# Kernel tuning notes

Measured on AMD Instinct MI355X. Metric: run time of the kernel, lower is better.

The kernel has to match this reference:

```python
import jax, jax.numpy as jnp
import numpy as np

B, C_IN, H, W = 4, 128, 32, 32
C_SKIP, C_OUT = 64, 64
D_MODEL = 2 * C_SKIP            # 128 (channels after concat)
D_STATE, D_CONV, EXPAND = 16, 4, 2
D_INNER = EXPAND * D_MODEL      # 256
DT_RANK = int(np.ceil(D_MODEL / 16))  # 8
LN_EPS = 1e-5


def setup_inputs() -> dict:
    key = jax.random.key(0)
    ks = jax.random.split(key, 12)
    s = 0.02
    return {
        "x": jax.random.normal(ks[0], (B, C_IN, H, W), jnp.float32),
        "skip_x": jax.random.normal(ks[1], (B, C_SKIP, 2 * H, 2 * W), jnp.float32),
        # ConvTranspose2d(in, skip, k=2, s=2): torch weight layout (in, out, kh, kw)
        "up_w": jax.random.normal(ks[2], (C_IN, C_SKIP, 2, 2), jnp.float32) * s,
        "up_b": jnp.zeros((C_SKIP,), jnp.float32),
        # Mamba params (torch Linear layout: (out_features, in_features))
        "in_proj_w": jax.random.normal(ks[3], (2 * D_INNER, D_MODEL), jnp.float32) * s,
        "conv1d_w": jax.random.normal(ks[4], (D_INNER, 1, D_CONV), jnp.float32) * s,
        "conv1d_b": jnp.zeros((D_INNER,), jnp.float32),
        "x_proj_w": jax.random.normal(ks[5], (DT_RANK + 2 * D_STATE, D_INNER), jnp.float32) * s,
        "dt_proj_w": jax.random.normal(ks[6], (D_INNER, DT_RANK), jnp.float32) * s,
        "dt_proj_b": jnp.zeros((D_INNER,), jnp.float32),
        "A_log": jnp.log(jnp.broadcast_to(jnp.arange(1, D_STATE + 1, dtype=jnp.float32), (D_INNER, D_STATE))),
        "Dp": jnp.ones((D_INNER,), jnp.float32),
        "out_proj_w": jax.random.normal(ks[7], (D_MODEL, D_INNER), jnp.float32) * s,
        "ln_gamma": jnp.ones((D_MODEL,), jnp.float32),
        "ln_beta": jnp.zeros((D_MODEL,), jnp.float32),
        # Conv2d 1x1 (out, in)
        "convout_w": jax.random.normal(ks[8], (C_OUT, D_MODEL), jnp.float32) * s,
        "convout_b": jnp.zeros((C_OUT,), jnp.float32),
    }


def _selective_scan(u, delta, A, Bm, Cm, Dp):
    # u, delta: (B,L,Din); A: (Din,Ds); Bm, Cm: (B,L,Ds)
    deltaA = jnp.exp(delta[..., None] * A)                        # (B,L,Din,Ds)
    deltaBu = delta[..., None] * Bm[:, :, None, :] * u[..., None]  # (B,L,Din,Ds)

    def step(h, xs):
        dA, dBu, c = xs                 # (B,Din,Ds),(B,Din,Ds),(B,Ds)
        h = dA * h + dBu
        y = jnp.einsum('bdn,bn->bd', h, c)
        return h, y

    h0 = jnp.zeros((u.shape[0], D_INNER, D_STATE), u.dtype)
    xs = (deltaA.transpose(1, 0, 2, 3), deltaBu.transpose(1, 0, 2, 3), Cm.transpose(1, 0, 2))
    _, ys = jax.lax.scan(step, h0, xs)  # (L,B,Din)
    return ys.transpose(1, 0, 2) + u * Dp


def _mamba(seq, in_proj_w, conv1d_w, conv1d_b, x_proj_w, dt_proj_w, dt_proj_b, A_log, Dp, out_proj_w):
    # seq: (B, L, D_MODEL)
    xz = seq @ in_proj_w.T                      # (B,L,2*Din)
    u, z = jnp.split(xz, 2, axis=-1)
    # depthwise causal conv1d along L
    uc = u.transpose(0, 2, 1)                   # (B,Din,L)
    uc = jax.lax.conv_general_dilated(
        uc, conv1d_w, window_strides=(1,), padding=[(D_CONV - 1, 0)],
        feature_group_count=D_INNER, dimension_numbers=('NCH', 'OIH', 'NCH'))
    uc = uc + conv1d_b[None, :, None]
    u = jax.nn.silu(uc.transpose(0, 2, 1))      # (B,L,Din)
    dbc = u @ x_proj_w.T                        # (B,L,DT_RANK+2*Ds)
    dt, Bm, Cm = jnp.split(dbc, [DT_RANK, DT_RANK + D_STATE], axis=-1)
    delta = jax.nn.softplus(dt @ dt_proj_w.T + dt_proj_b)
    A = -jnp.exp(A_log)
    y = _selective_scan(u, delta, A, Bm, Cm, Dp)
    y = y * jax.nn.silu(z)
    return y @ out_proj_w.T                     # (B,L,D_MODEL)


def reference(x, skip_x, up_w, up_b, in_proj_w, conv1d_w, conv1d_b, x_proj_w,
              dt_proj_w, dt_proj_b, A_log, Dp, out_proj_w, ln_gamma, ln_beta,
              convout_w, convout_b):
    b, _, h, w = x.shape
    # ConvTranspose2d k=2 s=2: each pixel expands to a 2x2 block
    up = jnp.einsum('bchw,coij->bohiwj', x, up_w).reshape(b, C_SKIP, 2 * h, 2 * w)
    up = up + up_b[None, :, None, None]
    xc = jnp.concatenate([up, skip_x], axis=1)  # (B, D_MODEL, 2H, 2W)
    Hh, Ww = xc.shape[2], xc.shape[3]
    seq = xc.reshape(b, D_MODEL, Hh * Ww).transpose(0, 2, 1)  # (B,L,D)
    y = _mamba(seq, in_proj_w, conv1d_w, conv1d_b, x_proj_w, dt_proj_w,
               dt_proj_b, A_log, Dp, out_proj_w)
    xm = y.transpose(0, 2, 1).reshape(b, D_MODEL, Hh, Ww)
    # permute -> LayerNorm over channels -> permute back
    xn = xm.transpose(0, 2, 3, 1)
    mu = xn.mean(-1, keepdims=True)
    var = xn.var(-1, keepdims=True)
    xn = (xn - mu) * jax.lax.rsqrt(var + LN_EPS) * ln_gamma + ln_beta
    xm = jax.nn.silu(xn.transpose(0, 3, 1, 2))
    out = jnp.einsum('bchw,oc->bohw', xm, convout_w) + convout_b[None, :, None, None]
    return out
```

## Files before the change

### kernel.cpp

```cpp
#include <hip/hip_runtime.h>

#define L_SEQ 4096
#define DM 128
#define DIN 256
#define NC 128
#define CHUNK 32

__global__ __launch_bounds__(256) void upcat_kernel(
    const float* __restrict__ x, const float* __restrict__ skip,
    const float* __restrict__ up_w, const float* __restrict__ up_b,
    float* __restrict__ seq) {
  int b = blockIdx.x >> 6, hh = blockIdx.x & 63;
  int h = hh >> 1, i = hh & 1;
  int tid = threadIdx.x;
  __shared__ float xs[128][32];
  __shared__ float wsh[2][128][64];
  for (int e = tid; e < 1024; e += 256) {
    int c = e >> 3, q = e & 7;
    *(float4*)&xs[c][q * 4] =
        *(const float4*)(x + (((size_t)b * 128 + c) * 32 + h) * 32 + q * 4);
  }
  for (int e = tid; e < 8192; e += 256) {
    int c = e >> 6, o = e & 63;
    float2 v = *(const float2*)(up_w + c * 256 + o * 4 + i * 2);
    wsh[0][c][o] = v.x;
    wsh[1][c][o] = v.y;
  }
  __syncthreads();
  int tx = tid & 15, ty = tid >> 4;
  float4 bv = *(const float4*)(up_b + tx * 4);
  float acc[4][4];
#pragma unroll
  for (int a = 0; a < 4; ++a) {
    acc[a][0] = bv.x; acc[a][1] = bv.y; acc[a][2] = bv.z; acc[a][3] = bv.w;
  }
#pragma unroll 4
  for (int c = 0; c < 128; ++c) {
    float x0 = xs[c][ty * 2];
    float x1 = xs[c][ty * 2 + 1];
    float4 w0 = *(const float4*)&wsh[0][c][tx * 4];
    float4 w1 = *(const float4*)&wsh[1][c][tx * 4];
    acc[0][0] = fmaf(x0, w0.x, acc[0][0]); acc[0][1] = fmaf(x0, w0.y, acc[0][1]);
    acc[0][2] = fmaf(x0, w0.z, acc[0][2]); acc[0][3] = fmaf(x0, w0.w, acc[0][3]);
    acc[1][0] = fmaf(x0, w1.x, acc[1][0]); acc[1][1] = fmaf(x0, w1.y, acc[1][1]);
    acc[1][2] = fmaf(x0, w1.z, acc[1][2]); acc[1][3] = fmaf(x0, w1.w, acc[1][3]);
    acc[2][0] = fmaf(x1, w0.x, acc[2][0]); acc[2][1] = fmaf(x1, w0.y, acc[2][1]);
    acc[2][2] = fmaf(x1, w0.z, acc[2][2]); acc[2][3] = fmaf(x1, w0.w, acc[2][3]);
    acc[3][0] = fmaf(x1, w1.x, acc[3][0]); acc[3][1] = fmaf(x1, w1.y, acc[3][1]);
    acc[3][2] = fmaf(x1, w1.z, acc[3][2]); acc[3][3] = fmaf(x1, w1.w, acc[3][3]);
  }
  size_t mrow_base = (size_t)b * L_SEQ + (size_t)hh * 64;
#pragma unroll
  for (int a = 0; a < 4; ++a) {
    int ww = ty * 4 + a;
    *(float4*)(seq + (mrow_base + ww) * DM + tx * 4) =
        make_float4(acc[a][0], acc[a][1], acc[a][2], acc[a][3]);
  }
  for (int e = tid; e < 4096; e += 256) {
    int c = e & 63, ww = e >> 6;
    seq[(mrow_base + ww) * DM + 64 + c] =
        skip[((size_t)b * 64 + c) * (size_t)L_SEQ + hh * 64 + ww];
  }
}

__global__ __launch_bounds__(256) void gemm_bt128(
    const float* __restrict__ A, const float* __restrict__ W,
    float* __restrict__ C, int M, int N, int K) {
  __shared__ float As[32][132];
  __shared__ float Ws[32][68];
  int m0 = blockIdx.x * 128, n0 = blockIdx.y * 64;
  int tid = threadIdx.x;
  int tx = tid & 15, ty = tid >> 4;
  float acc[8][4];
#pragma unroll
  for (int a = 0; a < 8; ++a)
#pragma unroll
    for (int bb = 0; bb < 4; ++bb) acc[a][bb] = 0.f;

  for (int k0 = 0; k0 < K; k0 += 32) {
    __syncthreads();
    for (int e = tid; e < 1024; e += 256) {
      int r = e >> 3, c4 = (e & 7) << 2;
      float4 va = *(const float4*)(A + (size_t)(m0 + r) * K + k0 + c4);
      As[c4 + 0][r] = va.x; As[c4 + 1][r] = va.y;
      As[c4 + 2][r] = va.z; As[c4 + 3][r] = va.w;
    }
    for (int e = tid; e < 512; e += 256) {
      int r = e >> 3, c4 = (e & 7) << 2;
      float4 vw = *(const float4*)(W + (size_t)(n0 + r) * K + k0 + c4);
      Ws[c4 + 0][r] = vw.x; Ws[c4 + 1][r] = vw.y;
      Ws[c4 + 2][r] = vw.z; Ws[c4 + 3][r] = vw.w;
    }
    __syncthreads();
#pragma unroll
    for (int kk = 0; kk < 32; ++kk) {
      float4 a0 = *(const float4*)(&As[kk][ty * 8]);
      float4 a1 = *(const float4*)(&As[kk][ty * 8 + 4]);
      float4 wv = *(const float4*)(&Ws[kk][tx * 4]);
      float a_[8] = {a0.x, a0.y, a0.z, a0.w, a1.x, a1.y, a1.z, a1.w};
      float w_[4] = {wv.x, wv.y, wv.z, wv.w};
#pragma unroll
      for (int a = 0; a < 8; ++a)
#pragma unroll
        for (int bb = 0; bb < 4; ++bb)
          acc[a][bb] = fmaf(a_[a], w_[bb], acc[a][bb]);
    }
  }
#pragma unroll
  for (int a = 0; a < 8; ++a)
#pragma unroll
    for (int bb = 0; bb < 4; ++bb)
      C[(size_t)(m0 + ty * 8 + a) * N + n0 + tx * 4 + bb] = acc[a][bb];
}

__global__ __launch_bounds__(256) void xproj_kernel(
    const float* __restrict__ xz, const float* __restrict__ cw,
    const float* __restrict__ cb, const float* __restrict__ W,
    float* __restrict__ dbc, float* __restrict__ u_out) {
  __shared__ float xzt[67][64];
  __shared__ float us[64][68];
  int m0 = blockIdx.x * 64;
  int tid = threadIdx.x;
  int lane = tid & 63;
  int w = __builtin_amdgcn_readfirstlane(tid >> 6);
  int jbase = blockIdx.y * 20 + w * 5;
  const float* Wb = W + jbase * 256;
  bool first = (m0 & (L_SEQ - 1)) == 0;
  int cc4 = (tid & 15) << 2;
  int r0 = tid >> 4;
  float acc[5];
#pragma unroll
  for (int j = 0; j < 5; ++j) acc[j] = 0.f;
  for (int k0 = 0; k0 < 256; k0 += 64) {
    __syncthreads();
    for (int e = tid; e < 67 * 16; e += 256) {
      int rr = e >> 4, c4 = (e & 15) << 2;
      float4 v;
      if (first && rr < 3)
        v = make_float4(0.f, 0.f, 0.f, 0.f);
      else
        v = *(const float4*)(xz + (size_t)(m0 - 3 + rr) * 512 + k0 + c4);
      *(float4*)&xzt[rr][c4] = v;
    }
    __syncthreads();
    {
      int d = k0 + cc4;
      float4 cw0 = *(const float4*)(cw + (d + 0) * 4);
      float4 cw1 = *(const float4*)(cw + (d + 1) * 4);
      float4 cw2 = *(const float4*)(cw + (d + 2) * 4);
      float4 cw3 = *(const float4*)(cw + (d + 3) * 4);
      float4 cbv = *(const float4*)(cb + d);
#pragma unroll
      for (int s = 0; s < 4; ++s) {
        int r = r0 + s * 16;
        float a0 = cbv.x, a1 = cbv.y, a2 = cbv.z, a3 = cbv.w;
        a0 = fmaf(xzt[r + 0][cc4 + 0], cw0.x, a0);
        a0 = fmaf(xzt[r + 1][cc4 + 0], cw0.y, a0);
        a0 = fmaf(xzt[r + 2][cc4 + 0], cw0.z, a0);
        a0 = fmaf(xzt[r + 3][cc4 + 0], cw0.w, a0);
        a1 = fmaf(xzt[r + 0][cc4 + 1], cw1.x, a1);
        a1 = fmaf(xzt[r + 1][cc4 + 1], cw1.y, a1);
        a1 = fmaf(xzt[r + 2][cc4 + 1], cw1.z, a1);
        a1 = fmaf(xzt[r + 3][cc4 + 1], cw1.w, a1);
        a2 = fmaf(xzt[r + 0][cc4 + 2], cw2.x, a2);
        a2 = fmaf(xzt[r + 1][cc4 + 2], cw2.y, a2);
        a2 = fmaf(xzt[r + 2][cc4 + 2], cw2.z, a2);
        a2 = fmaf(xzt[r + 3][cc4 + 2], cw2.w, a2);
        a3 = fmaf(xzt[r + 0][cc4 + 3], cw3.x, a3);
        a3 = fmaf(xzt[r + 1][cc4 + 3], cw3.y, a3);
        a3 = fmaf(xzt[r + 2][cc4 + 3], cw3.z, a3);
        a3 = fmaf(xzt[r + 3][cc4 + 3], cw3.w, a3);
        float o0 = a0 / (1.f + __expf(-a0));
        float o1 = a1 / (1.f + __expf(-a1));
        float o2 = a2 / (1.f + __expf(-a2));
        float o3 = a3 / (1.f + __expf(-a3));
        *(float4*)&us[r][cc4] = make_float4(o0, o1, o2, o3);
        if (blockIdx.y == 0)
          *(float4*)(u_out + (size_t)(m0 + r) * 256 + d) =
              make_float4(o0, o1, o2, o3);
      }
    }
    __syncthreads();
#pragma unroll
    for (int kk = 0; kk < 64; kk += 4) {
      float4 a4 = *(const float4*)&us[lane][kk];
      float a_[4] = {a4.x, a4.y, a4.z, a4.w};
#pragma unroll
      for (int i = 0; i < 4; ++i)
#pragma unroll
        for (int j = 0; j < 5; ++j)
          acc[j] = fmaf(a_[i], Wb[j * 256 + k0 + kk + i], acc[j]);
    }
  }
  size_t base = (size_t)(m0 + lane) * 40 + jbase;
#pragma unroll
  for (int j = 0; j < 5; ++j) dbc[base + j] = acc[j];
}

__device__ __forceinline__ float softplus_f(float a) {
  return (a > 20.f) ? a : log1pf(__expf(a));
}

__global__ __launch_bounds__(256) void scan_pass1(
    const float* __restrict__ u, const float* __restrict__ dbc,
    const float* __restrict__ A_log, const float* __restrict__ Wdt,
    const float* __restrict__ bdt, float* __restrict__ carryA,
    float* __restrict__ carryH) {
  int bid = blockIdx.x;
  int b = bid >> 7;
  int c = bid & (NC - 1);
  int d = threadIdx.x;
  __shared__ float ls[CHUNK * 40];
  size_t l0 = (size_t)b * L_SEQ + (size_t)c * CHUNK;
  const float* rp = dbc + l0 * 40;
  for (int e = d; e < CHUNK * 40; e += 256) ls[e] = rp[e];
  float Ac[16];
  {
    const float4* ar = (const float4*)(A_log + d * 16);
#pragma unroll
    for (int q = 0; q < 4; ++q) {
      float4 v = ar[q];
      Ac[q * 4 + 0] = -__expf(v.x); Ac[q * 4 + 1] = -__expf(v.y);
      Ac[q * 4 + 2] = -__expf(v.z); Ac[q * 4 + 3] = -__expf(v.w);
    }
  }
  float wdt[8];
  {
    const float4* wr = (const float4*)(Wdt + d * 8);
    float4 v0 = wr[0], v1 = wr[1];
    wdt[0] = v0.x; wdt[1] = v0.y; wdt[2] = v0.z; wdt[3] = v0.w;
    wdt[4] = v1.x; wdt[5] = v1.y; wdt[6] = v1.z; wdt[7] = v1.w;
  }
  float bdt_v = bdt[d];
  const float* up = u + l0 * 256 + d;
  __syncthreads();
  float h[16];
#pragma unroll
  for (int n = 0; n < 16; ++n) h[n] = 0.f;
  float dvs = 0.f;
#pragma unroll 4
  for (int li = 0; li < CHUNK; ++li) {
    float uv = up[(size_t)li * 256];
    float acc = bdt_v;
#pragma unroll
    for (int j = 0; j < 8; ++j)
      acc = fmaf(ls[li * 40 + j], wdt[j], acc);
    float dv = softplus_f(acc);
    dvs += dv;
    float t = dv * uv;
#pragma unroll
    for (int n = 0; n < 16; ++n) {
      float dA = __expf(dv * Ac[n]);
      h[n] = fmaf(dA, h[n], t * ls[li * 40 + 8 + n]);
    }
  }
  float4* cA = (float4*)(carryA + ((size_t)bid * 256 + d) * 16);
  float4* cH = (float4*)(carryH + ((size_t)bid * 256 + d) * 16);
#pragma unroll
  for (int q = 0; q < 4; ++q) {
    cA[q] = make_float4(__expf(dvs * Ac[q * 4]), __expf(dvs * Ac[q * 4 + 1]),
                        __expf(dvs * Ac[q * 4 + 2]), __expf(dvs * Ac[q * 4 + 3]));
    cH[q] = make_float4(h[q * 4], h[q * 4 + 1], h[q * 4 + 2], h[q * 4 + 3]);
  }
}

__global__ __launch_bounds__(64) void scan_mid(
    const float* __restrict__ carryA, float* __restrict__ carryH) {
  int gid = blockIdx.x * 64 + threadIdx.x;
  int b = gid >> 12;
  int dn = gid & 4095;
  size_t i = ((size_t)(b * NC) << 12) + dn;
  float h = 0.f;
  float a = carryA[i], hl = carryH[i];
#pragma unroll 4
  for (int c = 0; c < NC - 1; ++c) {
    size_t i2 = i + 4096;
    float a2 = carryA[i2];
    float hl2 = carryH[i2];
    carryH[i] = h;
    h = fmaf(a, h, hl);
    a = a2; hl = hl2; i = i2;
  }
  carryH[i] = h;
}

__global__ __launch_bounds__(256) void scan_pass3(
    const float* __restrict__ u, const float* __restrict__ dbc,
    const float* __restrict__ xz, const float* __restrict__ A_log,
    const float* __restrict__ Wdt, const float* __restrict__ bdt,
    const float* __restrict__ Dp, const float* __restrict__ carryH,
    float* __restrict__ y) {
  int bid = blockIdx.x;
  int b = bid >> 7;
  int c = bid & (NC - 1);
  int d = threadIdx.x;
  __shared__ float ls[CHUNK * 40];
  size_t l0 = (size_t)b * L_SEQ + (size_t)c * CHUNK;
  const float* rp = dbc + l0 * 40;
  for (int e = d; e < CHUNK * 40; e += 256) ls[e] = rp[e];
  float Ac[16];
  {
    const float4* ar = (const float4*)(A_log + d * 16);
#pragma unroll
    for (int q = 0; q < 4; ++q) {
      float4 v = ar[q];
      Ac[q * 4 + 0] = -__expf(v.x); Ac[q * 4 + 1] = -__expf(v.y);
      Ac[q * 4 + 2] = -__expf(v.z); Ac[q * 4 + 3] = -__expf(v.w);
    }
  }
  float wdt[8];
  {
    const float4* wr = (const float4*)(Wdt + d * 8);
    float4 v0 = wr[0], v1 = wr[1];
    wdt[0] = v0.x; wdt[1] = v0.y; wdt[2] = v0.z; wdt[3] = v0.w;
    wdt[4] = v1.x; wdt[5] = v1.y; wdt[6] = v1.z; wdt[7] = v1.w;
  }
  float bdt_v = bdt[d];
  float Dv = Dp[d];
  float h[16];
  {
    const float4* cH = (const float4*)(carryH + ((size_t)bid * 256 + d) * 16);
#pragma unroll
    for (int q = 0; q < 4; ++q) {
      float4 v = cH[q];
      h[q * 4 + 0] = v.x; h[q * 4 + 1] = v.y;
      h[q * 4 + 2] = v.z; h[q * 4 + 3] = v.w;
    }
  }
  const float* up = u + l0 * 256 + d;
  const float* zp = xz + l0 * 512 + 256 + d;
  float* yp = y + l0 * 256 + d;
  __syncthreads();
#pragma unroll 4
  for (int li = 0; li < CHUNK; ++li) {
    float uv = up[(size_t)li * 256];
    float zv = zp[(size_t)li * 512];
    float acc = bdt_v;
#pragma unroll
    for (int j = 0; j < 8; ++j)
      acc = fmaf(ls[li * 40 + j], wdt[j], acc);
    float dv = softplus_f(acc);
    float t = dv * uv;
    float p = 0.f;
#pragma unroll
    for (int n = 0; n < 16; ++n) {
      float dA = __expf(dv * Ac[n]);
      h[n] = fmaf(dA, h[n], t * ls[li * 40 + 8 + n]);
      p = fmaf(h[n], ls[li * 40 + 24 + n], p);
    }
    float s = zv / (1.f + __expf(-zv));
    yp[(size_t)li * 256] = (p + uv * Dv) * s;
  }
}

__global__ __launch_bounds__(512) void fused_out_kernel(
    const float* __restrict__ y, const float* __restrict__ Wp,
    const float* __restrict__ gamma, const float* __restrict__ beta,
    const float* __restrict__ Wo, const float* __restrict__ bo,
    float* __restrict__ out) {
  __shared__ float As[32][68];
  __shared__ float Ws[32][132];
  __shared__ float xt[64][129];
  __shared__ float mus[64], invs[64];
  int tid = threadIdx.x;
  int m0 = blockIdx.x * 64;
  int tx = tid & 31, ty = tid >> 5;
  float acc[4][4];
#pragma unroll
  for (int a = 0; a < 4; ++a)
#pragma unroll
    for (int bb = 0; bb < 4; ++bb) acc[a][bb] = 0.f;

  for (int k0 = 0; k0 < 256; k0 += 32) {
    __syncthreads();
    {
      int e = tid;
      int r = e >> 3, c4 = (e & 7) << 2;
      float4 va = *(const float4*)(y + (size_t)(m0 + r) * 256 + k0 + c4);
      As[c4 + 0][r] = va.x; As[c4 + 1][r] = va.y;
      As[c4 + 2][r] = va.z; As[c4 + 3][r] = va.w;
    }
    for (int e = tid; e < 1024; e += 512) {
      int n = e >> 3, c4 = (e & 7) << 2;
      float4 vw = *(const float4*)(Wp + (size_t)n * 256 + k0 + c4);
      Ws[c4 + 0][n] = vw.x; Ws[c4 + 1][n] = vw.y;
      Ws[c4 + 2][n] = vw.z; Ws[c4 + 3][n] = vw.w;
    }
    __syncthreads();
#pragma unroll
    for (int kk = 0; kk < 32; ++kk) {
      float4 av = *(const float4*)(&As[kk][ty * 4]);
      float4 wv = *(const float4*)(&Ws[kk][tx * 4]);
      float a_[4] = {av.x, av.y, av.z, av.w};
      float w_[4] = {wv.x, wv.y, wv.z, wv.w};
#pragma unroll
      for (int a = 0; a < 4; ++a)
#pragma unroll
        for (int bb = 0; bb < 4; ++bb)
          acc[a][bb] = fmaf(a_[a], w_[bb], acc[a][bb]);
    }
  }
  __syncthreads();
#pragma unroll
  for (int a = 0; a < 4; ++a)
    *(float4*)&xt[ty * 4 + a][tx * 4] =
        make_float4(acc[a][0], acc[a][1], acc[a][2], acc[a][3]);
  __syncthreads();
  {
    int r = tid >> 3, kq = (tid & 7) * 16;
    float s = 0.f, q = 0.f;
#pragma unroll 8
    for (int kk = 0; kk < 16; ++kk) {
      float v = xt[r][kq + kk];
      s += v; q = fmaf(v, v, q);
    }
    s += __shfl_xor(s, 1, 64); s += __shfl_xor(s, 2, 64);
    s += __shfl_xor(s, 4, 64);
    q += __shfl_xor(q, 1, 64); q += __shfl_xor(q, 2, 64);
    q += __shfl_xor(q, 4, 64);
    if ((tid & 7) == 0) {
      float mu = s * (1.f / 128.f);
      float var = q * (1.f / 128.f) - mu * mu;
      mus[r] = mu;
      invs[r] = rsqrtf(var + 1e-5f);
    }
  }
  __syncthreads();
  for (int i = 0; i < 16; ++i) {
    int idx = tid + i * 512;
    int r = idx >> 7, k = idx & 127;
    float v = xt[r][k];
    float xn = (v - mus[r]) * invs[r] * gamma[k] + beta[k];
    xt[r][k] = xn / (1.f + __expf(-xn));
  }
  __syncthreads();
  int lane = tid & 63;
  int w = __builtin_amdgcn_readfirstlane(tid >> 6);
  int cbase = w * 8;
  const float* Wrow = Wo + cbase * 128;
  float acc2[8];
#pragma unroll
  for (int j = 0; j < 8; ++j) acc2[j] = 0.f;
#pragma unroll 4
  for (int k = 0; k < 128; ++k) {
    float v = xt[lane][k];
#pragma unroll
    for (int j = 0; j < 8; ++j)
      acc2[j] = fmaf(v, Wrow[j * 128 + k], acc2[j]);
  }
  int m = m0 + lane;
  int b = m >> 12, l = m & 4095;
#pragma unroll
  for (int j = 0; j < 8; ++j)
    out[((size_t)b * 64 + cbase + j) * 4096 + l] = acc2[j] + bo[cbase + j];
}

extern "C" void kernel_launch(void* const* d_in, const int* in_sizes, int n_in,
                              void* d_out, int out_size, void* d_ws, size_t ws_size,
                              hipStream_t stream) {
  (void)in_sizes; (void)n_in; (void)out_size; (void)ws_size;
  const float* x         = (const float*)d_in[0];
  const float* skip      = (const float*)d_in[1];
  const float* up_w      = (const float*)d_in[2];
  const float* up_b      = (const float*)d_in[3];
  const float* in_proj_w = (const float*)d_in[4];
  const float* conv1d_w  = (const float*)d_in[5];
  const float* conv1d_b  = (const float*)d_in[6];
  const float* x_proj_w  = (const float*)d_in[7];
  const float* dt_proj_w = (const float*)d_in[8];
  const float* dt_proj_b = (const float*)d_in[9];
  const float* A_log     = (const float*)d_in[10];
  const float* Dp        = (const float*)d_in[11];
  const float* out_proj_w= (const float*)d_in[12];
  const float* ln_gamma  = (const float*)d_in[13];
  const float* ln_beta   = (const float*)d_in[14];
  const float* convout_w = (const float*)d_in[15];
  const float* convout_b = (const float*)d_in[16];
  float* out = (float*)d_out;
  float* ws  = (float*)d_ws;

  float* seq    = ws;
  float* xz     = ws + 2097152;
  float* u      = ws + 10485760;
  float* dbc    = ws + 14680064;
  float* y      = ws + 15335424;
  float* carryA = ws + 19529728;
  float* carryH = ws + 21626880;

  upcat_kernel<<<256, 256, 0, stream>>>(x, skip, up_w, up_b, seq);
  gemm_bt128<<<dim3(16384 / 128, 512 / 64), 256, 0, stream>>>(
      seq, in_proj_w, xz, 16384, 512, 128);
  xproj_kernel<<<dim3(16384 / 64, 2), 256, 0, stream>>>(
      xz, conv1d_w, conv1d_b, x_proj_w, dbc, u);
  scan_pass1<<<4 * NC, 256, 0, stream>>>(u, dbc, A_log, dt_proj_w, dt_proj_b,
                                         carryA, carryH);
  scan_mid<<<256, 64, 0, stream>>>(carryA, carryH);
  scan_pass3<<<4 * NC, 256, 0, stream>>>(u, dbc, xz, A_log, dt_proj_w,
                                         dt_proj_b, Dp, carryH, y);
  fused_out_kernel<<<256, 512, 0, stream>>>(y, out_proj_w, ln_gamma, ln_beta,
                                            convout_w, convout_b, out);
}
```

Baseline: 201.5 us.

## Replace tiled SGEMMs with wave-uniform scalar-weight GEMMs for in_proj and out_proj

Both the in_proj GEMM and the out_proj part of the fused output kernel now use the same scheme. Each lane owns one row, whose activations are staged in LDS, and each wave owns 16 output columns whose weights are read as wave-uniform (scalar) loads. This removes the transposed LDS stores and the per-k-tile weight staging. The in_proj output goes through an LDS tile so the global stores stay coalesced. The trade-off is lower register blocking per thread (16 outputs against one activation per k), so arithmetic intensity per LDS read drops, which the scalar weight loads are meant to offset.

```diff
diff --git a/kernel.cpp b/kernel.cpp
--- a/kernel.cpp
+++ b/kernel.cpp
@@ -63,54 +63,47 @@
   }
 }
 
-__global__ __launch_bounds__(256) void gemm_bt128(
-    const float* __restrict__ A, const float* __restrict__ W,
-    float* __restrict__ C, int M, int N, int K) {
-  __shared__ float As[32][132];
-  __shared__ float Ws[32][68];
-  int m0 = blockIdx.x * 128, n0 = blockIdx.y * 64;
+__global__ __launch_bounds__(512) void inproj_kernel(
+    const float* __restrict__ seq, const float* __restrict__ W,
+    float* __restrict__ xz) {
+  __shared__ float us[64][133];
+  __shared__ float ot[64][129];
+  int m0 = blockIdx.x * 64;
+  int cb0 = blockIdx.y * 128;
   int tid = threadIdx.x;
-  int tx = tid & 15, ty = tid >> 4;
-  float acc[8][4];
-#pragma unroll
-  for (int a = 0; a < 8; ++a)
-#pragma unroll
-    for (int bb = 0; bb < 4; ++bb) acc[a][bb] = 0.f;
-
-  for (int k0 = 0; k0 < K; k0 += 32) {
-    __syncthreads();
-    for (int e = tid; e < 1024; e += 256) {
-      int r = e >> 3, c4 = (e & 7) << 2;
-      float4 va = *(const float4*)(A + (size_t)(m0 + r) * K + k0 + c4);
-      As[c4 + 0][r] = va.x; As[c4 + 1][r] = va.y;
-      As[c4 + 2][r] = va.z; As[c4 + 3][r] = va.w;
-    }
-    for (int e = tid; e < 512; e += 256) {
-      int r = e >> 3, c4 = (e & 7) << 2;
-      float4 vw = *(const float4*)(W + (size_t)(n0 + r) * K + k0 + c4);
-      Ws[c4 + 0][r] = vw.x; Ws[c4 + 1][r] = vw.y;
-      Ws[c4 + 2][r] = vw.z; Ws[c4 + 3][r] = vw.w;
-    }
-    __syncthreads();
-#pragma unroll
-    for (int kk = 0; kk < 32; ++kk) {
-      float4 a0 = *(const float4*)(&As[kk][ty * 8]);
-      float4 a1 = *(const float4*)(&As[kk][ty * 8 + 4]);
-      float4 wv = *(const float4*)(&Ws[kk][tx * 4]);
-      float a_[8] = {a0.x, a0.y, a0.z, a0.w, a1.x, a1.y, a1.z, a1.w};
-      float w_[4] = {wv.x, wv.y, wv.z, wv.w};
-#pragma unroll
-      for (int a = 0; a < 8; ++a)
-#pragma unroll
-        for (int bb = 0; bb < 4; ++bb)
-          acc[a][bb] = fmaf(a_[a], w_[bb], acc[a][bb]);
-    }
-  }
-#pragma unroll
-  for (int a = 0; a < 8; ++a)
-#pragma unroll
-    for (int bb = 0; bb < 4; ++bb)
-      C[(size_t)(m0 + ty * 8 + a) * N + n0 + tx * 4 + bb] = acc[a][bb];
+  int lane = tid & 63;
+  int w = __builtin_amdgcn_readfirstlane(tid >> 6);
+  const float* Wrow = W + (size_t)(cb0 + w * 16) * 128;
+#pragma unroll
+  for (int i = 0; i < 4; ++i) {
+    int e = tid + i * 512;
+    int r = e >> 5, cq = e & 31;
+    *(float4*)&us[r][cq * 4] =
+        *(const float4*)(seq + (size_t)(m0 + r) * 128 + cq * 4);
+  }
+  __syncthreads();
+  float acc[16];
+#pragma unroll
+  for (int j = 0; j < 16; ++j) acc[j] = 0.f;
+#pragma unroll 4
+  for (int k = 0; k < 128; ++k) {
+    float v = us[lane][k];
+#pragma unroll
+    for (int j = 0; j < 16; ++j)
+      acc[j] = fmaf(v, Wrow[j * 128 + k], acc[j]);
+  }
+#pragma unroll
+  for (int q = 0; q < 4; ++q)
+    *(float4*)&ot[lane][w * 16 + q * 4] =
+        make_float4(acc[q * 4], acc[q * 4 + 1], acc[q * 4 + 2], acc[q * 4 + 3]);
+  __syncthreads();
+#pragma unroll
+  for (int i = 0; i < 4; ++i) {
+    int e = tid + i * 512;
+    int r = e >> 5, cq = e & 31;
+    *(float4*)(xz + (size_t)(m0 + r) * 512 + cb0 + cq * 4) =
+        *(const float4*)&ot[r][cq * 4];
+  }
 }
 
 __global__ __launch_bounds__(256) void xproj_kernel(
@@ -358,53 +351,40 @@
     const float* __restrict__ gamma, const float* __restrict__ beta,
     const float* __restrict__ Wo, const float* __restrict__ bo,
     float* __restrict__ out) {
-  __shared__ float As[32][68];
-  __shared__ float Ws[32][132];
+  __shared__ float us[64][133];
   __shared__ float xt[64][129];
   __shared__ float mus[64], invs[64];
   int tid = threadIdx.x;
   int m0 = blockIdx.x * 64;
-  int tx = tid & 31, ty = tid >> 5;
-  float acc[4][4];
-#pragma unroll
-  for (int a = 0; a < 4; ++a)
-#pragma unroll
-    for (int bb = 0; bb < 4; ++bb) acc[a][bb] = 0.f;
-
-  for (int k0 = 0; k0 < 256; k0 += 32) {
+  int lane = tid & 63;
+  int w = __builtin_amdgcn_readfirstlane(tid >> 6);
+  float acc[16];
+#pragma unroll
+  for (int j = 0; j < 16; ++j) acc[j] = 0.f;
+  for (int kc = 0; kc < 256; kc += 128) {
     __syncthreads();
-    {
-      int e = tid;
-      int r = e >> 3, c4 = (e & 7) << 2;
-      float4 va = *(const float4*)(y + (size_t)(m0 + r) * 256 + k0 + c4);
-      As[c4 + 0][r] = va.x; As[c4 + 1][r] = va.y;
-      As[c4 + 2][r] = va.z; As[c4 + 3][r] = va.w;
-    }
-    for (int e = tid; e < 1024; e += 512) {
-      int n = e >> 3, c4 = (e & 7) << 2;
-      float4 vw = *(const float4*)(Wp + (size_t)n * 256 + k0 + c4);
-      Ws[c4 + 0][n] = vw.x; Ws[c4 + 1][n] = vw.y;
-      Ws[c4 + 2][n] = vw.z; Ws[c4 + 3][n] = vw.w;
+#pragma unroll
+    for (int i = 0; i < 4; ++i) {
+      int e = tid + i * 512;
+      int r = e >> 5, cq = e & 31;
+      *(float4*)&us[r][cq * 4] =
+          *(const float4*)(y + (size_t)(m0 + r) * 256 + kc + cq * 4);
     }
     __syncthreads();
-#pragma unroll
-    for (int kk = 0; kk < 32; ++kk) {
-      float4 av = *(const float4*)(&As[kk][ty * 4]);
-      float4 wv = *(const float4*)(&Ws[kk][tx * 4]);
-      float a_[4] = {av.x, av.y, av.z, av.w};
-      float w_[4] = {wv.x, wv.y, wv.z, wv.w};
-#pragma unroll
-      for (int a = 0; a < 4; ++a)
-#pragma unroll
-        for (int bb = 0; bb < 4; ++bb)
-          acc[a][bb] = fmaf(a_[a], w_[bb], acc[a][bb]);
-    }
-  }
-  __syncthreads();
-#pragma unroll
-  for (int a = 0; a < 4; ++a)
-    *(float4*)&xt[ty * 4 + a][tx * 4] =
-        make_float4(acc[a][0], acc[a][1], acc[a][2], acc[a][3]);
+    const float* Wrow = Wp + (size_t)(w * 16) * 256 + kc;
+#pragma unroll 4
+    for (int k = 0; k < 128; ++k) {
+      float v = us[lane][k];
+#pragma unroll
+      for (int j = 0; j < 16; ++j)
+        acc[j] = fmaf(v, Wrow[j * 256 + k], acc[j]);
+    }
+  }
+  __syncthreads();
+#pragma unroll
+  for (int q = 0; q < 4; ++q)
+    *(float4*)&xt[lane][w * 16 + q * 4] =
+        make_float4(acc[q * 4], acc[q * 4 + 1], acc[q * 4 + 2], acc[q * 4 + 3]);
   __syncthreads();
   {
     int r = tid >> 3, kq = (tid & 7) * 16;
@@ -434,10 +414,8 @@
     xt[r][k] = xn / (1.f + __expf(-xn));
   }
   __syncthreads();
-  int lane = tid & 63;
-  int w = __builtin_amdgcn_readfirstlane(tid >> 6);
   int cbase = w * 8;
-  const float* Wrow = Wo + cbase * 128;
+  const float* Wrow2 = Wo + cbase * 128;
   float acc2[8];
 #pragma unroll
   for (int j = 0; j < 8; ++j) acc2[j] = 0.f;
@@ -446,7 +424,7 @@
     float v = xt[lane][k];
 #pragma unroll
     for (int j = 0; j < 8; ++j)
-      acc2[j] = fmaf(v, Wrow[j * 128 + k], acc2[j]);
+      acc2[j] = fmaf(v, Wrow2[j * 128 + k], acc2[j]);
   }
   int m = m0 + lane;
   int b = m >> 12, l = m & 4095;
@@ -488,8 +466,7 @@
   float* carryH = ws + 21626880;
 
   upcat_kernel<<<256, 256, 0, stream>>>(x, skip, up_w, up_b, seq);
-  gemm_bt128<<<dim3(16384 / 128, 512 / 64), 256, 0, stream>>>(
-      seq, in_proj_w, xz, 16384, 512, 128);
+  inproj_kernel<<<dim3(16384 / 64, 4), 512, 0, stream>>>(seq, in_proj_w, xz);
   xproj_kernel<<<dim3(16384 / 64, 2), 256, 0, stream>>>(
       xz, conv1d_w, conv1d_b, x_proj_w, dbc, u);
   scan_pass1<<<4 * NC, 256, 0, stream>>>(u, dbc, A_log, dt_proj_w, dt_proj_b,
```

New measurement: 224.9 us. +11.6%, slower.
